# Performance work log

Measured on AMD Instinct MI355X. Metric: run time of the kernel, lower is better.

## Reference

```python
import jax, jax.numpy as jnp
import numpy as np

HEADS = 4
HID = 610
KER = 50  # cov2KerSize
NEG_SLOPE = 0.2


def gat_layer(x, src, dst, w, b, att_src, att_dst, n_nodes):
    # x: [N, Fin], w: [HEADS*HID, Fin], att_*: [1, HEADS, HID], b: [HID]
    h = (x @ w.T).reshape(n_nodes, HEADS, HID)               # [N,H,D]
    a_src = (h * att_src).sum(-1)                            # [N,H]
    a_dst = (h * att_dst).sum(-1)                            # [N,H]
    alpha = jax.nn.leaky_relu(a_src[src] + a_dst[dst], NEG_SLOPE)  # [E,H]
    # softmax over edges grouped by destination node
    m = jax.ops.segment_max(alpha, dst, num_segments=n_nodes)
    e = jnp.exp(alpha - m[dst])
    denom = jax.ops.segment_sum(e, dst, num_segments=n_nodes)
    a = e / (denom[dst] + 1e-16)                             # [E,H]
    msg = h[src] * a[:, :, None]                             # [E,H,D]
    out = jax.ops.segment_sum(msg, dst, num_segments=n_nodes)  # [N,H,D]
    return out.mean(axis=1) + b                              # [N,D] (concat=False)


def setup_inputs() -> dict:
    key = jax.random.key(0)
    ks = jax.random.split(key, 16)
    N, E, FIN, NOUT = 20000, 100000, 128, 86
    x = jax.random.normal(ks[0], (N, FIN), dtype=jnp.float32)
    edge_index = jax.random.randint(ks[1], (2, E), 0, N, dtype=jnp.int64)
    def kaiming(k, shape, fan_in):
        return jax.random.normal(k, shape, dtype=jnp.float32) * np.float32(np.sqrt(2.0 / fan_in))
    w0 = kaiming(ks[2], (HEADS * HID, FIN), FIN)
    b0 = jnp.zeros((HID,), jnp.float32)
    att_src0 = kaiming(ks[3], (1, HEADS, HID), HID)
    att_dst0 = kaiming(ks[4], (1, HEADS, HID), HID)
    w2 = kaiming(ks[5], (HEADS * HID, HID), HID)
    b2 = jnp.zeros((HID,), jnp.float32)
    att_src1 = kaiming(ks[6], (1, HEADS, HID), HID)
    att_dst1 = kaiming(ks[7], (1, HEADS, HID), HID)
    w4 = kaiming(ks[8], (1, 1, 2, KER), 2 * KER)
    b4 = jnp.zeros((1,), jnp.float32)
    w6 = kaiming(ks[9], (1, 1, KER), KER)
    b6 = jnp.zeros((1,), jnp.float32)
    w8 = kaiming(ks[10], (NOUT, 512), 512)
    b8 = jnp.zeros((NOUT,), jnp.float32)
    return dict(x=x, edge_index=edge_index, w0=w0, b0=b0, att_src0=att_src0,
                att_dst0=att_dst0, w2=w2, b2=b2, att_src1=att_src1,
                att_dst1=att_dst1, w4=w4, b4=b4, w6=w6, b6=b6, w8=w8, b8=b8)


def reference(x, edge_index, w0, b0, att_src0, att_dst0, w2, b2, att_src1,
              att_dst1, w4, b4, w6, b6, w8, b8):
    N = x.shape[0]
    src, dst = edge_index[0], edge_index[1]
    x1 = jax.nn.relu(gat_layer(x, src, dst, w0, b0, att_src0, att_dst0, N))
    x2 = jax.nn.relu(gat_layer(x1, src, dst, w2, b2, att_src1, att_dst1, N))
    # edge features: cat(src_feat, dst_feat) viewed as [E,1,2,HID]
    ef = jnp.stack([x2[src], x2[dst]], axis=1)[:, None, :, :]  # [E,1,2,HID]
    y = jax.lax.conv_general_dilated(ef, w4, (1, 1), 'VALID',
                                     dimension_numbers=('NCHW', 'OIHW', 'NCHW'))
    y = jax.nn.relu(y + b4[None, :, None, None])               # [E,1,1,561]
    y = y.reshape(-1, HID - KER + 1, 1).transpose(0, 2, 1)     # [E,1,561]
    y = jax.lax.conv_general_dilated(y, w6, (1,), 'VALID',
                                     dimension_numbers=('NCH', 'OIH', 'NCH'))
    y = jax.nn.relu(y + b6[None, :, None])                     # [E,1,512]
    # adaptive_avg_pool1d to 512 is identity since length is already 512
    y = y.reshape(-1, 512)
    return y @ w8.T + b8                                       # [E, num_outputs]
```

## Files before the change

kernel.cpp:

```cpp
#include <hip/hip_runtime.h>
#include <math.h>

#define HEADS 4
#define HID 610
#define HIDP 640
#define FIN 128
#define KER 50
#define NOUT 86
#define NEG_SLOPE 0.2f

#define Y1S 616
#define ZSS 520

typedef short bf8_t __attribute__((ext_vector_type(8)));
typedef float f4_t __attribute__((ext_vector_type(4)));

__device__ __forceinline__ ushort f2bf(float f) {
    unsigned u = __float_as_uint(f);
    unsigned r = (u + 0x7FFFu + ((u >> 16) & 1u)) >> 16;
    return (ushort)r;
}
__device__ __forceinline__ ushort f2bf_t(float f) {
    return (ushort)(__float_as_uint(f) >> 16);
}
__device__ __forceinline__ float bf2f(ushort b) { return __uint_as_float(((unsigned)b) << 16); }

__global__ void fill_val(float* __restrict__ p, float v, long n) {
    long i = (long)blockIdx.x * blockDim.x + threadIdx.x;
    if (i < n) p[i] = v;
}

__global__ void copy_int(const int* __restrict__ a, int* __restrict__ b, int n) {
    int i = blockIdx.x * blockDim.x + threadIdx.x;
    if (i < n) b[i] = a[i];
}

__global__ void hist_k(const int* __restrict__ ei, int* __restrict__ hist, int E) {
    int e = blockIdx.x * blockDim.x + threadIdx.x;
    if (e < E) atomicAdd(&hist[ei[E + e]], 1);
}

__global__ __launch_bounds__(1024) void scan_k(const int* __restrict__ hist,
                                               int* __restrict__ base, int Nn) {
    __shared__ int tmp[1024];
    __shared__ int carry;
    if (threadIdx.x == 0) carry = 0;
    __syncthreads();
    for (int c0 = 0; c0 < Nn; c0 += 1024) {
        int i = c0 + threadIdx.x;
        int v = (i < Nn) ? hist[i] : 0;
        tmp[threadIdx.x] = v;
        __syncthreads();
        for (int off = 1; off < 1024; off <<= 1) {
            int t = (threadIdx.x >= off) ? tmp[threadIdx.x - off] : 0;
            __syncthreads();
            tmp[threadIdx.x] += t;
            __syncthreads();
        }
        if (i < Nn) base[i] = carry + tmp[threadIdx.x] - v;
        __syncthreads();
        if (threadIdx.x == 1023) carry += tmp[1023];
        __syncthreads();
    }
    if (threadIdx.x == 0) base[Nn] = carry;
}

__global__ void scatter_k(const int* __restrict__ ei, int* __restrict__ cursor,
                          int* __restrict__ esrc, int E) {
    int e = blockIdx.x * blockDim.x + threadIdx.x;
    if (e >= E) return;
    int d = ei[E + e];
    int pos = atomicAdd(&cursor[d], 1);
    esrc[pos] = ei[e];
}

__global__ void split_pad(const float* __restrict__ in, ushort* __restrict__ hi,
                          ushort* __restrict__ lo, int R, int K, int Kp) {
    long i = (long)blockIdx.x * blockDim.x + threadIdx.x;
    if (i >= (long)R * Kp) return;
    int r = (int)(i / Kp), c = (int)(i % Kp);
    float v = (c < K) ? in[(long)r * K + c] : 0.f;
    ushort h = f2bf(v);
    hi[i] = h;
    lo[i] = f2bf(v - bf2f(h));
}

__global__ void build_toeplitz(const float* __restrict__ w4, const float* __restrict__ w6,
                               ushort* __restrict__ T) {
    int i = blockIdx.x * blockDim.x + threadIdx.x;
    if (i >= 18 * 512) return;
    int e = i & 7;
    int lane = (i >> 3) & 63;
    int f = i >> 9;
    int n = lane & 15;
    int k = ((lane >> 4) << 3) + e;
    float wv;
    int hilo;
    if (f < 12) {
        int c = f % 3, hc = f / 3;
        int ch = hc & 1;
        hilo = hc >> 1;
        int d = c * 32 + k - n;
        wv = (d >= 0 && d < KER) ? w4[ch * KER + d] : 0.f;
    } else {
        int r2 = f - 12;
        int c = r2 % 3;
        hilo = r2 / 3;
        int d = c * 32 + k - n;
        wv = (d >= 0 && d < KER) ? w6[d] : 0.f;
    }
    ushort h = f2bf(wv);
    T[i] = hilo ? f2bf(wv - bf2f(h)) : h;
}

template <int AMODE, bool BIAS>
__global__ __launch_bounds__(256) void gemm_mfma(const float* __restrict__ A,
                                                 const ushort* __restrict__ Aghi,
                                                 const ushort* __restrict__ Aglo,
                                                 const ushort* __restrict__ Bghi,
                                                 const ushort* __restrict__ Bglo,
                                                 const float* __restrict__ bias,
                                                 float* __restrict__ C,
                                                 int M, int N, int Kp) {
    __shared__ __align__(16) ushort Ah[128 * 32];
    __shared__ __align__(16) ushort Al[128 * 32];
    __shared__ __align__(16) ushort Bh[128 * 32];
    __shared__ __align__(16) ushort Bl[128 * 32];
    int tid = threadIdx.x;
    int wave = tid >> 6, lane = tid & 63;
    int quad = lane >> 4, l16 = lane & 15;
    int wm = wave & 1, wn = wave >> 1;
    int row0 = blockIdx.y * 128, col0 = blockIdx.x * 128;

    float4 pa0[4];
    uint4 pah[2], pal[2], pbh[2], pbl[2];

    auto loadA = [&](int k0) {
        if (AMODE == 0) {
#pragma unroll
            for (int q = 0; q < 4; q++) {
                int p = tid + q * 256;
                int r = p >> 3, c4 = (p & 7) << 2;
                int gr = row0 + r;
                pa0[q] = (gr < M) ? *(const float4*)(A + (size_t)gr * Kp + k0 + c4)
                                  : make_float4(0.f, 0.f, 0.f, 0.f);
            }
        } else {
#pragma unroll
            for (int q = 0; q < 2; q++) {
                int p = tid + q * 256;
                int r = p >> 2, c = p & 3;
                int gr = row0 + r;
                if (gr < M) {
                    pah[q] = *(const uint4*)(Aghi + (size_t)gr * Kp + k0 + c * 8);
                    pal[q] = *(const uint4*)(Aglo + (size_t)gr * Kp + k0 + c * 8);
                } else {
                    pah[q] = make_uint4(0, 0, 0, 0);
                    pal[q] = make_uint4(0, 0, 0, 0);
                }
            }
        }
    };
    auto loadB = [&](int k0) {
#pragma unroll
        for (int q = 0; q < 2; q++) {
            int p = tid + q * 256;
            int r = p >> 2, c = p & 3;
            int gr = col0 + r;
            if (gr < N) {
                pbh[q] = *(const uint4*)(Bghi + (size_t)gr * Kp + k0 + c * 8);
                pbl[q] = *(const uint4*)(Bglo + (size_t)gr * Kp + k0 + c * 8);
            } else {
                pbh[q] = make_uint4(0, 0, 0, 0);
                pbl[q] = make_uint4(0, 0, 0, 0);
            }
        }
    };
    auto writeLDS = [&]() {
        if (AMODE == 0) {
#pragma unroll
            for (int q = 0; q < 4; q++) {
                int p = tid + q * 256;
                int r = p >> 3, m = p & 7;
                int pos = r * 32 + ((((m >> 1)) ^ ((r >> 1) & 3)) << 3) + ((m & 1) << 2);
                float4 v = pa0[q];
                ushort4 hv, lv;
                hv.x = f2bf(v.x); lv.x = f2bf(v.x - bf2f(hv.x));
                hv.y = f2bf(v.y); lv.y = f2bf(v.y - bf2f(hv.y));
                hv.z = f2bf(v.z); lv.z = f2bf(v.z - bf2f(hv.z));
                hv.w = f2bf(v.w); lv.w = f2bf(v.w - bf2f(hv.w));
                *(ushort4*)&Ah[pos] = hv;
                *(ushort4*)&Al[pos] = lv;
            }
        } else {
#pragma unroll
            for (int q = 0; q < 2; q++) {
                int p = tid + q * 256;
                int r = p >> 2, c = p & 3;
                int pos = r * 32 + ((c ^ ((r >> 1) & 3)) << 3);
                *(uint4*)&Ah[pos] = pah[q];
                *(uint4*)&Al[pos] = pal[q];
            }
        }
#pragma unroll
        for (int q = 0; q < 2; q++) {
            int p = tid + q * 256;
            int r = p >> 2, c = p & 3;
            int pos = r * 32 + ((c ^ ((r >> 1) & 3)) << 3);
            *(uint4*)&Bh[pos] = pbh[q];
            *(uint4*)&Bl[pos] = pbl[q];
        }
    };

    f4_t acc[4][4];
#pragma unroll
    for (int i = 0; i < 4; i++)
#pragma unroll
        for (int j = 0; j < 4; j++) acc[i][j] = (f4_t){0.f, 0.f, 0.f, 0.f};

    loadA(0);
    loadB(0);
    int sw = (quad ^ ((l16 >> 1) & 3)) << 3;
    for (int k0 = 0; k0 < Kp; k0 += 32) {
        __syncthreads();
        writeLDS();
        __syncthreads();
        if (k0 + 32 < Kp) {
            loadA(k0 + 32);
            loadB(k0 + 32);
        }
        bf8_t ah[4], al[4], bh[4], bl[4];
#pragma unroll
        for (int t = 0; t < 4; t++) {
            int ar = wm * 64 + t * 16 + l16;
            ah[t] = *(const bf8_t*)&Ah[ar * 32 + sw];
            al[t] = *(const bf8_t*)&Al[ar * 32 + sw];
            int br = wn * 64 + t * 16 + l16;
            bh[t] = *(const bf8_t*)&Bh[br * 32 + sw];
            bl[t] = *(const bf8_t*)&Bl[br * 32 + sw];
        }
#pragma unroll
        for (int i = 0; i < 4; i++)
#pragma unroll
            for (int j = 0; j < 4; j++) {
                acc[i][j] = __builtin_amdgcn_mfma_f32_16x16x32_bf16(ah[i], bh[j], acc[i][j], 0, 0, 0);
                acc[i][j] = __builtin_amdgcn_mfma_f32_16x16x32_bf16(al[i], bh[j], acc[i][j], 0, 0, 0);
                acc[i][j] = __builtin_amdgcn_mfma_f32_16x16x32_bf16(ah[i], bl[j], acc[i][j], 0, 0, 0);
            }
    }
#pragma unroll
    for (int i = 0; i < 4; i++) {
#pragma unroll
        for (int r = 0; r < 4; r++) {
            int grow = row0 + wm * 64 + i * 16 + quad * 4 + r;
            if (grow >= M) continue;
#pragma unroll
            for (int j = 0; j < 4; j++) {
                int gcol = col0 + wn * 64 + j * 16 + l16;
                if (gcol >= N) continue;
                float v = acc[i][j][r];
                if (BIAS) v += bias[gcol];
                C[(size_t)grow * N + gcol] = v;
            }
        }
    }
}

__global__ __launch_bounds__(256) void attn_dots(const float* __restrict__ h,
                                                 const float* __restrict__ att_s,
                                                 const float* __restrict__ att_d,
                                                 float* __restrict__ a_src,
                                                 float* __restrict__ a_dst, int Nn) {
    int n = blockIdx.x;
    int head = threadIdx.x >> 6;
    int lane = threadIdx.x & 63;
    const float2* hr = (const float2*)(h + (long)n * (HEADS * HID) + head * HID);
    const float2* as = (const float2*)(att_s + head * HID);
    const float2* ad = (const float2*)(att_d + head * HID);
    float ss = 0.f, sd = 0.f;
    for (int d = lane; d < HID / 2; d += 64) {
        float2 hv = hr[d], av = as[d], dv = ad[d];
        ss += hv.x * av.x + hv.y * av.y;
        sd += hv.x * dv.x + hv.y * dv.y;
    }
    for (int off = 32; off > 0; off >>= 1) {
        ss += __shfl_down(ss, off);
        sd += __shfl_down(sd, off);
    }
    if (lane == 0) {
        a_src[n * HEADS + head] = ss;
        a_dst[n * HEADS + head] = sd;
    }
}

template <int OUTMODE>
__global__ __launch_bounds__(256) void node_aggregate(
    const float* __restrict__ h, const float* __restrict__ asrc,
    const float* __restrict__ adst, const int* __restrict__ base,
    const int* __restrict__ esrc, const float* __restrict__ bias,
    float* __restrict__ xout, ushort* __restrict__ xhi, ushort* __restrict__ xlo,
    int Nn) {
    int wave = threadIdx.x >> 6, lane = threadIdx.x & 63;
    int n = blockIdx.x * 4 + wave;
    if (n >= Nn) return;
    int b0 = base[n], deg = base[n + 1] - b0;
    float ad[HEADS];
#pragma unroll
    for (int hh = 0; hh < HEADS; hh++) ad[hh] = adst[n * HEADS + hh];
    float m[HEADS] = {-INFINITY, -INFINITY, -INFINITY, -INFINITY};
    for (int eb = 0; eb < deg; eb += 64) {
        int i = eb + lane;
        if (i < deg) {
            int s = esrc[b0 + i];
#pragma unroll
            for (int hh = 0; hh < HEADS; hh++) {
                float v = asrc[s * HEADS + hh] + ad[hh];
                v = v >= 0.f ? v : NEG_SLOPE * v;
                m[hh] = fmaxf(m[hh], v);
            }
        }
    }
#pragma unroll
    for (int off = 32; off > 0; off >>= 1)
#pragma unroll
        for (int hh = 0; hh < HEADS; hh++) m[hh] = fmaxf(m[hh], __shfl_xor(m[hh], off));
    float sden[HEADS] = {0.f, 0.f, 0.f, 0.f};
    for (int eb = 0; eb < deg; eb += 64) {
        int i = eb + lane;
        if (i < deg) {
            int s = esrc[b0 + i];
#pragma unroll
            for (int hh = 0; hh < HEADS; hh++) {
                float v = asrc[s * HEADS + hh] + ad[hh];
                v = v >= 0.f ? v : NEG_SLOPE * v;
                sden[hh] += expf(v - m[hh]);
            }
        }
    }
#pragma unroll
    for (int off = 32; off > 0; off >>= 1)
#pragma unroll
        for (int hh = 0; hh < HEADS; hh++) sden[hh] += __shfl_xor(sden[hh], off);
    float inv[HEADS];
#pragma unroll
    for (int hh = 0; hh < HEADS; hh++) inv[hh] = 0.25f / (sden[hh] + 1e-16f);
    float acc0[10] = {}, acc1[10] = {}, acc2[10] = {}, acc3[10] = {};
    for (int eb = 0; eb < deg; eb += 64) {
        int i = eb + lane;
        int sreg = 0;
        float coef[HEADS] = {0.f, 0.f, 0.f, 0.f};
        if (i < deg) {
            sreg = esrc[b0 + i];
#pragma unroll
            for (int hh = 0; hh < HEADS; hh++) {
                float v = asrc[sreg * HEADS + hh] + ad[hh];
                v = v >= 0.f ? v : NEG_SLOPE * v;
                coef[hh] = expf(v - m[hh]) * inv[hh];
            }
        }
        int cnt = deg - eb < 64 ? deg - eb : 64;
        for (int j = 0; j < cnt; j++) {
            int s = __shfl(sreg, j);
            float c0 = __shfl(coef[0], j), c1 = __shfl(coef[1], j);
            float c2 = __shfl(coef[2], j), c3 = __shfl(coef[3], j);
            const float* hr = h + (size_t)s * (HEADS * HID);
#pragma unroll
            for (int t = 0; t < 10; t++) {
                int d = lane + t * 64;
                if (d < HID) {
                    acc0[t] = fmaf(c0, hr[d], acc0[t]);
                    acc1[t] = fmaf(c1, hr[HID + d], acc1[t]);
                    acc2[t] = fmaf(c2, hr[2 * HID + d], acc2[t]);
                    acc3[t] = fmaf(c3, hr[3 * HID + d], acc3[t]);
                }
            }
        }
    }
#pragma unroll
    for (int t = 0; t < 10; t++) {
        int d = lane + t * 64;
        if (d < HID) {
            float v = acc0[t] + acc1[t] + acc2[t] + acc3[t] + bias[d];
            v = v > 0.f ? v : 0.f;
            if (OUTMODE == 0) {
                xout[(size_t)n * HIDP + d] = v;
            } else {
                ushort hv = f2bf(v);
                xhi[(size_t)n * HIDP + d] = hv;
                xlo[(size_t)n * HIDP + d] = f2bf(v - bf2f(hv));
            }
        }
    }
    for (int d = HID + lane; d < HIDP; d += 64) {
        if (OUTMODE == 0) {
            xout[(size_t)n * HIDP + d] = 0.f;
        } else {
            xhi[(size_t)n * HIDP + d] = 0;
            xlo[(size_t)n * HIDP + d] = 0;
        }
    }
}

__global__ __launch_bounds__(256, 2) void edge_fused(
    const ushort* __restrict__ x2hi, const ushort* __restrict__ x2lo,
    const int* __restrict__ ei, const ushort* __restrict__ T,
    const float* __restrict__ b4, const float* __restrict__ b6,
    const ushort* __restrict__ w8hi, const ushort* __restrict__ w8lo,
    const float* __restrict__ b8, float* __restrict__ out, int E) {
    __shared__ __align__(16) ushort y1h[32 * Y1S];
    __shared__ __align__(16) ushort y1l[32 * Y1S];
    const int tid = threadIdx.x;
    const int wave = tid >> 6, lane = tid & 63;
    const int quad = lane >> 4, l16 = lane & 15;
    const int e0 = blockIdx.x * 32;
    const int et = wave & 1;
    const int jb0 = wave >> 1;

    for (int i = tid; i < 32 * (Y1S - 576); i += 256) {
        int r = i / (Y1S - 576);
        int j = 576 + (i - r * (Y1S - 576));
        y1h[r * Y1S + j] = 0;
        y1l[r * Y1S + j] = 0;
    }

    bf8_t B1h[2][3], B1l[2][3];
#pragma unroll
    for (int ch = 0; ch < 2; ch++)
#pragma unroll
        for (int c = 0; c < 3; c++) {
            B1h[ch][c] = *(const bf8_t*)&T[(ch * 3 + c) * 512 + lane * 8];
            B1l[ch][c] = *(const bf8_t*)&T[((2 + ch) * 3 + c) * 512 + lane * 8];
        }

    int eidx = e0 + et * 16 + l16;
    if (eidx >= E) eidx = E - 1;
    const ushort* psh = x2hi + (size_t)ei[eidx] * HIDP + quad * 8;
    const ushort* psl = x2lo + (size_t)ei[eidx] * HIDP + quad * 8;
    const ushort* pth = x2hi + (size_t)ei[E + eidx] * HIDP + quad * 8;
    const ushort* ptl = x2lo + (size_t)ei[E + eidx] * HIDP + quad * 8;
    const float bb4 = b4[0], bb6 = b6[0];

    bf8_t pre0[12], pre1[12];
    auto ldA = [&](bf8_t(&dst)[12], int jb) {
        const int o_ = jb * 16;
#pragma unroll
        for (int c = 0; c < 3; c++) {
            dst[c * 4 + 0] = *(const bf8_t*)(psh + o_ + c * 32);
            dst[c * 4 + 1] = *(const bf8_t*)(psl + o_ + c * 32);
            dst[c * 4 + 2] = *(const bf8_t*)(pth + o_ + c * 32);
            dst[c * 4 + 3] = *(const bf8_t*)(ptl + o_ + c * 32);
        }
    };
    auto conv1_tile = [&](const bf8_t(&A)[12], int jb) {
        const int j0 = jb * 16;
        f4_t acc = {bb4, bb4, bb4, bb4};
#pragma unroll
        for (int c = 0; c < 3; c++) {
            acc = __builtin_amdgcn_mfma_f32_16x16x32_bf16(A[c * 4 + 0], B1h[0][c], acc, 0, 0, 0);
            acc = __builtin_amdgcn_mfma_f32_16x16x32_bf16(A[c * 4 + 1], B1h[0][c], acc, 0, 0, 0);
            acc = __builtin_amdgcn_mfma_f32_16x16x32_bf16(A[c * 4 + 0], B1l[0][c], acc, 0, 0, 0);
            acc = __builtin_amdgcn_mfma_f32_16x16x32_bf16(A[c * 4 + 2], B1h[1][c], acc, 0, 0, 0);
            acc = __builtin_amdgcn_mfma_f32_16x16x32_bf16(A[c * 4 + 3], B1h[1][c], acc, 0, 0, 0);
            acc = __builtin_amdgcn_mfma_f32_16x16x32_bf16(A[c * 4 + 2], B1l[1][c], acc, 0, 0, 0);
        }
#pragma unroll
        for (int r = 0; r < 4; r++) {
            int e_ = et * 16 + quad * 4 + r;
            int pos = e_ * Y1S + j0 + l16;
            float v = acc[r];
            v = v > 0.f ? v : 0.f;
            ushort hh = f2bf_t(v);
            y1h[pos] = hh;
            y1l[pos] = f2bf(v - bf2f(hh));
        }
    };

    ldA(pre0, jb0);
    for (int tt = 0; tt < 9; tt++) {
        int jbA = jb0 + 4 * tt;
        ldA(pre1, jbA + 2);
        conv1_tile(pre0, jbA);
        if (tt < 8) ldA(pre0, jbA + 4);
        conv1_tile(pre1, jbA + 2);
    }
    __syncthreads();

    bf8_t B2h[3], B2l[3];
#pragma unroll
    for (int c = 0; c < 3; c++) {
        B2h[c] = *(const bf8_t*)&T[(12 + c) * 512 + lane * 8];
        B2l[c] = *(const bf8_t*)&T[(15 + c) * 512 + lane * 8];
    }
    const int arow1 = (et * 16 + l16) * Y1S + quad * 8;
    f4_t zac[16];
#pragma unroll
    for (int t = 0; t < 16; t++) {
        const int j02 = (jb0 + 2 * t) * 16;
        f4_t acc = {bb6, bb6, bb6, bb6};
#pragma unroll
        for (int c = 0; c < 3; c++) {
            bf8_t ah = *(const bf8_t*)&y1h[arow1 + j02 + c * 32];
            bf8_t al = *(const bf8_t*)&y1l[arow1 + j02 + c * 32];
            acc = __builtin_amdgcn_mfma_f32_16x16x32_bf16(ah, B2h[c], acc, 0, 0, 0);
            acc = __builtin_amdgcn_mfma_f32_16x16x32_bf16(al, B2h[c], acc, 0, 0, 0);
            acc = __builtin_amdgcn_mfma_f32_16x16x32_bf16(ah, B2l[c], acc, 0, 0, 0);
        }
#pragma unroll
        for (int r = 0; r < 4; r++) {
            float v = acc[r];
            zac[t][r] = v > 0.f ? v : 0.f;
        }
    }
    __syncthreads();

#pragma unroll
    for (int t = 0; t < 16; t++) {
        const int j02 = (jb0 + 2 * t) * 16;
#pragma unroll
        for (int r = 0; r < 4; r++) {
            int e_ = et * 16 + quad * 4 + r;
            int pos = e_ * ZSS + j02 + l16;
            float v = zac[t][r];
            ushort hh = f2bf_t(v);
            y1h[pos] = hh;
            y1l[pos] = f2bf(v - bf2f(hh));
        }
    }
    __syncthreads();

#pragma unroll
    for (int it = 0; it < 3; it++) {
        const int item = wave + it * 4;
        const int et2 = item & 1, nt = item >> 1;
        const int col = nt * 16 + l16;
        const int wrow = col < NOUT ? col : 0;
        const float bias = col < NOUT ? b8[col] : 0.f;
        f4_t acc = {bias, bias, bias, bias};
        const int arow = (et2 * 16 + l16) * ZSS + quad * 8;
        const ushort* wph = w8hi + (size_t)wrow * 512 + quad * 8;
        const ushort* wpl = w8lo + (size_t)wrow * 512 + quad * 8;
#pragma unroll
        for (int c = 0; c < 16; c++) {
            bf8_t zh = *(const bf8_t*)&y1h[arow + c * 32];
            bf8_t zl = *(const bf8_t*)&y1l[arow + c * 32];
            bf8_t wh = *(const bf8_t*)(wph + c * 32);
            bf8_t wl = *(const bf8_t*)(wpl + c * 32);
            acc = __builtin_amdgcn_mfma_f32_16x16x32_bf16(zh, wh, acc, 0, 0, 0);
            acc = __builtin_amdgcn_mfma_f32_16x16x32_bf16(zl, wh, acc, 0, 0, 0);
            acc = __builtin_amdgcn_mfma_f32_16x16x32_bf16(zh, wl, acc, 0, 0, 0);
        }
        if (col < NOUT) {
#pragma unroll
            for (int r = 0; r < 4; r++) {
                int e_ = e0 + et2 * 16 + quad * 4 + r;
                if (e_ < E) out[(size_t)e_ * NOUT + col] = acc[r];
            }
        }
    }
}

extern "C" void kernel_launch(void* const* d_in, const int* in_sizes, int n_in,
                              void* d_out, int out_size, void* d_ws, size_t ws_size,
                              hipStream_t stream) {
    const float* x = (const float*)d_in[0];
    const int* ei = (const int*)d_in[1];
    const float* w0 = (const float*)d_in[2];
    const float* b0 = (const float*)d_in[3];
    const float* att_s0 = (const float*)d_in[4];
    const float* att_d0 = (const float*)d_in[5];
    const float* w2 = (const float*)d_in[6];
    const float* b2 = (const float*)d_in[7];
    const float* att_s1 = (const float*)d_in[8];
    const float* att_d1 = (const float*)d_in[9];
    const float* w4 = (const float*)d_in[10];
    const float* b4 = (const float*)d_in[11];
    const float* w6 = (const float*)d_in[12];
    const float* b6 = (const float*)d_in[13];
    const float* w8 = (const float*)d_in[14];
    const float* b8 = (const float*)d_in[15];
    float* out = (float*)d_out;

    const int Nn = in_sizes[0] / FIN;
    const int E = in_sizes[1] / 2;
    const int HD = HEADS * HID;

    float* ws = (float*)d_ws;
    size_t o = 0;
    float* buf1 = ws + o; o += (size_t)Nn * HIDP;
    ushort* x1hi = (ushort*)buf1;
    ushort* x1lo = x1hi + (size_t)Nn * HIDP;
    ushort* w8hi = (ushort*)(ws + o);
    ushort* w8lo = w8hi + (size_t)NOUT * 512; o += (size_t)NOUT * 512;
    int* base = (int*)(ws + o); o += (size_t)Nn + 4;
    int* cursor = (int*)(ws + o); o += (size_t)Nn;
    int* esrc = (int*)(ws + o); o += (size_t)E;
    float* asrc = ws + o; o += (size_t)Nn * HEADS;
    float* adst = ws + o; o += (size_t)Nn * HEADS;
    ushort* w0hi = (ushort*)(ws + o);
    ushort* w0lo = w0hi + (size_t)HD * FIN; o += (size_t)HD * FIN;
    ushort* w2hi = (ushort*)(ws + o);
    ushort* w2lo = w2hi + (size_t)HD * HIDP; o += (size_t)HD * HIDP;
    float* h = ws + o;

    int edgeGrid = (E + 255) / 256;
    int nodeWaveGrid = (Nn + 3) / 4;
    int fusedGrid = (E + 31) / 32;
    dim3 gGemmL((HD + 127) / 128, (Nn + 127) / 128);

    split_pad<<<((HD * FIN) + 255) / 256, 256, 0, stream>>>(w0, w0hi, w0lo, HD, FIN, FIN);
    split_pad<<<((HD * HIDP) + 255) / 256, 256, 0, stream>>>(w2, w2hi, w2lo, HD, HID, HIDP);
    split_pad<<<((NOUT * 512) + 255) / 256, 256, 0, stream>>>(w8, w8hi, w8lo, NOUT, 512, 512);
    fill_val<<<(Nn + 255) / 256, 256, 0, stream>>>((float*)cursor, 0.f, Nn);
    hist_k<<<edgeGrid, 256, 0, stream>>>(ei, cursor, E);
    scan_k<<<1, 1024, 0, stream>>>(cursor, base, Nn);
    copy_int<<<(Nn + 255) / 256, 256, 0, stream>>>(base, cursor, Nn);
    scatter_k<<<edgeGrid, 256, 0, stream>>>(ei, cursor, esrc, E);

    gemm_mfma<0, false><<<gGemmL, 256, 0, stream>>>(x, nullptr, nullptr, w0hi, w0lo, nullptr,
                                                    h, Nn, HD, FIN);
    build_toeplitz<<<(18 * 512 + 255) / 256, 256, 0, stream>>>(w4, w6, w0hi);
    attn_dots<<<Nn, 256, 0, stream>>>(h, att_s0, att_d0, asrc, adst, Nn);
    node_aggregate<1><<<nodeWaveGrid, 256, 0, stream>>>(h, asrc, adst, base, esrc, b0,
                                                        nullptr, x1hi, x1lo, Nn);

    gemm_mfma<1, false><<<gGemmL, 256, 0, stream>>>(nullptr, x1hi, x1lo, w2hi, w2lo, nullptr,
                                                    h, Nn, HD, HIDP);
    attn_dots<<<Nn, 256, 0, stream>>>(h, att_s1, att_d1, asrc, adst, Nn);
    node_aggregate<1><<<nodeWaveGrid, 256, 0, stream>>>(h, asrc, adst, base, esrc, b2,
                                                        nullptr, x1hi, x1lo, Nn);

    edge_fused<<<fusedGrid, 256, 0, stream>>>(x1hi, x1lo, ei, w0hi, b4, b6,
                                              w8hi, w8lo, b8, out, E);
}
```

Baseline: 1.282 ms.

## Reuse overlapping conv input chunks in a register ring and drop zero-weight MFMAs

The conv1 and conv2 stages in the edge kernel now keep a rotating ring of input chunks in registers. Consecutive output tiles that share overlapping 32-wide windows reuse loaded data instead of reloading three chunks per tile from global or LDS. It also drops the lo-part MFMAs for the third kernel chunk, where the Toeplitz weight residual is presumably zero or negligible, cutting MFMA count per tile from 18 to 14 (conv1) and 9 to 7 (conv2). The ring is held in many live vector registers, which raises register pressure and may hurt occupancy under launch_bounds(256,2).

After: 1.091 ms. 1.18x faster.

```diff
diff --git a/kernel.cpp b/kernel.cpp
--- a/kernel.cpp
+++ b/kernel.cpp
@@ -414,23 +414,8 @@
     const int quad = lane >> 4, l16 = lane & 15;
     const int e0 = blockIdx.x * 32;
     const int et = wave & 1;
-    const int jb0 = wave >> 1;
-
-    for (int i = tid; i < 32 * (Y1S - 576); i += 256) {
-        int r = i / (Y1S - 576);
-        int j = 576 + (i - r * (Y1S - 576));
-        y1h[r * Y1S + j] = 0;
-        y1l[r * Y1S + j] = 0;
-    }
-
-    bf8_t B1h[2][3], B1l[2][3];
-#pragma unroll
-    for (int ch = 0; ch < 2; ch++)
-#pragma unroll
-        for (int c = 0; c < 3; c++) {
-            B1h[ch][c] = *(const bf8_t*)&T[(ch * 3 + c) * 512 + lane * 8];
-            B1l[ch][c] = *(const bf8_t*)&T[((2 + ch) * 3 + c) * 512 + lane * 8];
-        }
+    const int p = wave >> 1;
+    const int p16 = p * 16;
 
     int eidx = e0 + et * 16 + l16;
     if (eidx >= E) eidx = E - 1;
@@ -438,31 +423,60 @@
     const ushort* psl = x2lo + (size_t)ei[eidx] * HIDP + quad * 8;
     const ushort* pth = x2hi + (size_t)ei[E + eidx] * HIDP + quad * 8;
     const ushort* ptl = x2lo + (size_t)ei[E + eidx] * HIDP + quad * 8;
+
+    bf8_t Wsh[8], Wsl[8], Wth[8], Wtl[8];
+#define LDCH(slot, m)                                     \
+    {                                                     \
+        const int o_ = p16 + 32 * (m);                    \
+        Wsh[slot] = *(const bf8_t*)(psh + o_);            \
+        Wth[slot] = *(const bf8_t*)(pth + o_);            \
+        if ((m) <= 18) {                                  \
+            Wsl[slot] = *(const bf8_t*)(psl + o_);        \
+            Wtl[slot] = *(const bf8_t*)(ptl + o_);        \
+        }                                                 \
+    }
+#pragma unroll
+    for (int m = 0; m < 7; m++) LDCH(m, m);
+
+    for (int i = tid; i < 32 * (Y1S - 576); i += 256) {
+        int r = i / (Y1S - 576);
+        int j = 576 + (i - r * (Y1S - 576));
+        y1h[r * Y1S + j] = 0;
+        y1l[r * Y1S + j] = 0;
+    }
+
+    bf8_t B1h[2][3], B1l[2][2];
+#pragma unroll
+    for (int ch = 0; ch < 2; ch++) {
+#pragma unroll
+        for (int c = 0; c < 3; c++)
+            B1h[ch][c] = *(const bf8_t*)&T[(ch * 3 + c) * 512 + lane * 8];
+#pragma unroll
+        for (int c = 0; c < 2; c++)
+            B1l[ch][c] = *(const bf8_t*)&T[((2 + ch) * 3 + c) * 512 + lane * 8];
+    }
     const float bb4 = b4[0], bb6 = b6[0];
 
-    bf8_t pre0[12], pre1[12];
-    auto ldA = [&](bf8_t(&dst)[12], int jb) {
-        const int o_ = jb * 16;
-#pragma unroll
-        for (int c = 0; c < 3; c++) {
-            dst[c * 4 + 0] = *(const bf8_t*)(psh + o_ + c * 32);
-            dst[c * 4 + 1] = *(const bf8_t*)(psl + o_ + c * 32);
-            dst[c * 4 + 2] = *(const bf8_t*)(pth + o_ + c * 32);
-            dst[c * 4 + 3] = *(const bf8_t*)(ptl + o_ + c * 32);
-        }
-    };
-    auto conv1_tile = [&](const bf8_t(&A)[12], int jb) {
-        const int j0 = jb * 16;
+#pragma unroll
+    for (int t = 0; t < 18; t++) {
+        if (t <= 12) LDCH((t + 7) & 7, t + 7);
+        const int c0 = t & 7, c1 = (t + 1) & 7, c2 = (t + 2) & 7;
         f4_t acc = {bb4, bb4, bb4, bb4};
-#pragma unroll
-        for (int c = 0; c < 3; c++) {
-            acc = __builtin_amdgcn_mfma_f32_16x16x32_bf16(A[c * 4 + 0], B1h[0][c], acc, 0, 0, 0);
-            acc = __builtin_amdgcn_mfma_f32_16x16x32_bf16(A[c * 4 + 1], B1h[0][c], acc, 0, 0, 0);
-            acc = __builtin_amdgcn_mfma_f32_16x16x32_bf16(A[c * 4 + 0], B1l[0][c], acc, 0, 0, 0);
-            acc = __builtin_amdgcn_mfma_f32_16x16x32_bf16(A[c * 4 + 2], B1h[1][c], acc, 0, 0, 0);
-            acc = __builtin_amdgcn_mfma_f32_16x16x32_bf16(A[c * 4 + 3], B1h[1][c], acc, 0, 0, 0);
-            acc = __builtin_amdgcn_mfma_f32_16x16x32_bf16(A[c * 4 + 2], B1l[1][c], acc, 0, 0, 0);
-        }
+        acc = __builtin_amdgcn_mfma_f32_16x16x32_bf16(Wsh[c0], B1h[0][0], acc, 0, 0, 0);
+        acc = __builtin_amdgcn_mfma_f32_16x16x32_bf16(Wsl[c0], B1h[0][0], acc, 0, 0, 0);
+        acc = __builtin_amdgcn_mfma_f32_16x16x32_bf16(Wsh[c0], B1l[0][0], acc, 0, 0, 0);
+        acc = __builtin_amdgcn_mfma_f32_16x16x32_bf16(Wth[c0], B1h[1][0], acc, 0, 0, 0);
+        acc = __builtin_amdgcn_mfma_f32_16x16x32_bf16(Wtl[c0], B1h[1][0], acc, 0, 0, 0);
+        acc = __builtin_amdgcn_mfma_f32_16x16x32_bf16(Wth[c0], B1l[1][0], acc, 0, 0, 0);
+        acc = __builtin_amdgcn_mfma_f32_16x16x32_bf16(Wsh[c1], B1h[0][1], acc, 0, 0, 0);
+        acc = __builtin_amdgcn_mfma_f32_16x16x32_bf16(Wsl[c1], B1h[0][1], acc, 0, 0, 0);
+        acc = __builtin_amdgcn_mfma_f32_16x16x32_bf16(Wsh[c1], B1l[0][1], acc, 0, 0, 0);
+        acc = __builtin_amdgcn_mfma_f32_16x16x32_bf16(Wth[c1], B1h[1][1], acc, 0, 0, 0);
+        acc = __builtin_amdgcn_mfma_f32_16x16x32_bf16(Wtl[c1], B1h[1][1], acc, 0, 0, 0);
+        acc = __builtin_amdgcn_mfma_f32_16x16x32_bf16(Wth[c1], B1l[1][1], acc, 0, 0, 0);
+        acc = __builtin_amdgcn_mfma_f32_16x16x32_bf16(Wsh[c2], B1h[0][2], acc, 0, 0, 0);
+        acc = __builtin_amdgcn_mfma_f32_16x16x32_bf16(Wth[c2], B1h[1][2], acc, 0, 0, 0);
+        const int j0 = p16 + 32 * t;
 #pragma unroll
         for (int r = 0; r < 4; r++) {
             int e_ = et * 16 + quad * 4 + r;
@@ -473,38 +487,37 @@
             y1h[pos] = hh;
             y1l[pos] = f2bf(v - bf2f(hh));
         }
-    };
-
-    ldA(pre0, jb0);
-    for (int tt = 0; tt < 9; tt++) {
-        int jbA = jb0 + 4 * tt;
-        ldA(pre1, jbA + 2);
-        conv1_tile(pre0, jbA);
-        if (tt < 8) ldA(pre0, jbA + 4);
-        conv1_tile(pre1, jbA + 2);
     }
     __syncthreads();
 
-    bf8_t B2h[3], B2l[3];
-#pragma unroll
-    for (int c = 0; c < 3; c++) {
-        B2h[c] = *(const bf8_t*)&T[(12 + c) * 512 + lane * 8];
-        B2l[c] = *(const bf8_t*)&T[(15 + c) * 512 + lane * 8];
-    }
+    bf8_t B2h[3], B2l[2];
+#pragma unroll
+    for (int c = 0; c < 3; c++) B2h[c] = *(const bf8_t*)&T[(12 + c) * 512 + lane * 8];
+#pragma unroll
+    for (int c = 0; c < 2; c++) B2l[c] = *(const bf8_t*)&T[(15 + c) * 512 + lane * 8];
     const int arow1 = (et * 16 + l16) * Y1S + quad * 8;
+    bf8_t Yh[4], Yl[4];
+#define LDY(slot, m)                                          \
+    {                                                         \
+        const int o_ = arow1 + p16 + 32 * (m);                \
+        Yh[slot] = *(const bf8_t*)&y1h[o_];                   \
+        if ((m) <= 16) Yl[slot] = *(const bf8_t*)&y1l[o_];    \
+    }
+#pragma unroll
+    for (int m = 0; m < 3; m++) LDY(m, m);
     f4_t zac[16];
 #pragma unroll
     for (int t = 0; t < 16; t++) {
-        const int j02 = (jb0 + 2 * t) * 16;
+        if (t <= 14) LDY((t + 3) & 3, t + 3);
+        const int c0 = t & 3, c1 = (t + 1) & 3, c2 = (t + 2) & 3;
         f4_t acc = {bb6, bb6, bb6, bb6};
-#pragma unroll
-        for (int c = 0; c < 3; c++) {
-            bf8_t ah = *(const bf8_t*)&y1h[arow1 + j02 + c * 32];
-            bf8_t al = *(const bf8_t*)&y1l[arow1 + j02 + c * 32];
-            acc = __builtin_amdgcn_mfma_f32_16x16x32_bf16(ah, B2h[c], acc, 0, 0, 0);
-            acc = __builtin_amdgcn_mfma_f32_16x16x32_bf16(al, B2h[c], acc, 0, 0, 0);
-            acc = __builtin_amdgcn_mfma_f32_16x16x32_bf16(ah, B2l[c], acc, 0, 0, 0);
-        }
+        acc = __builtin_amdgcn_mfma_f32_16x16x32_bf16(Yh[c0], B2h[0], acc, 0, 0, 0);
+        acc = __builtin_amdgcn_mfma_f32_16x16x32_bf16(Yl[c0], B2h[0], acc, 0, 0, 0);
+        acc = __builtin_amdgcn_mfma_f32_16x16x32_bf16(Yh[c0], B2l[0], acc, 0, 0, 0);
+        acc = __builtin_amdgcn_mfma_f32_16x16x32_bf16(Yh[c1], B2h[1], acc, 0, 0, 0);
+        acc = __builtin_amdgcn_mfma_f32_16x16x32_bf16(Yl[c1], B2h[1], acc, 0, 0, 0);
+        acc = __builtin_amdgcn_mfma_f32_16x16x32_bf16(Yh[c1], B2l[1], acc, 0, 0, 0);
+        acc = __builtin_amdgcn_mfma_f32_16x16x32_bf16(Yh[c2], B2h[2], acc, 0, 0, 0);
 #pragma unroll
         for (int r = 0; r < 4; r++) {
             float v = acc[r];
@@ -515,7 +528,7 @@
 
 #pragma unroll
     for (int t = 0; t < 16; t++) {
-        const int j02 = (jb0 + 2 * t) * 16;
+        const int j02 = p16 + 32 * t;
 #pragma unroll
         for (int r = 0; r < 4; r++) {
             int e_ = et * 16 + quad * 4 + r;
@@ -557,6 +570,8 @@
             }
         }
     }
+#undef LDCH
+#undef LDY
 }
 
 extern "C" void kernel_launch(void* const* d_in, const int* in_sizes, int n_in,
```
